# Performance work log

Hardware: AMD Instinct MI355X
Metric: run time of the kernel (lower is better)

The kernel has to match this reference:

```python
import jax, jax.numpy as jnp
import numpy as np

N, F, E, C = 50000, 128, 800000, 10

def setup_inputs() -> dict:
    key = jax.random.key(0)
    ks = jax.random.split(key, 16)
    s = 1.0 / np.sqrt(F)
    def u(k, shape):
        return jax.random.uniform(k, shape, jnp.float32, -s, s)
    inp = {
        "x": jax.random.normal(ks[0], (N, F), jnp.float32),
        "edge_index": jax.random.randint(ks[1], (2, E), 0, N),
    }
    for i, p in enumerate(["1", "2"]):
        b = 2 + i * 5
        inp["W" + p] = u(ks[b], (F, F))          # EvolveGCNO initial_weight
        inp["wih" + p] = u(ks[b + 1], (3 * F, F))  # GRU input weights (r,z,n)
        inp["whh" + p] = u(ks[b + 2], (3 * F, F))  # GRU hidden weights
        inp["bih" + p] = u(ks[b + 3], (3 * F,))
        inp["bhh" + p] = u(ks[b + 4], (3 * F,))
    inp["lin_w"] = u(ks[12], (C, F))
    inp["lin_b"] = u(ks[13], (C,))
    return inp

def gru_step(x, h, wih, whh, bih, bhh):
    # torch.nn.GRU single step; gate order r, z, n
    gi = x @ wih.T + bih
    gh = h @ whh.T + bhh
    ir, iz, inn = jnp.split(gi, 3, axis=-1)
    hr, hz, hn = jnp.split(gh, 3, axis=-1)
    r = jax.nn.sigmoid(ir + hr)
    z = jax.nn.sigmoid(iz + hz)
    n = jnp.tanh(inn + r * hn)
    return (1.0 - z) * n + z * h

def gcn_conv(W, x, src, dst):
    # GCNConv_Fixed_W: gcn_norm with self-loops, then aggregate (x @ W)
    n = x.shape[0]
    loop = jnp.arange(n)
    s = jnp.concatenate([src, loop])
    d = jnp.concatenate([dst, loop])
    deg = jax.ops.segment_sum(jnp.ones(s.shape[0], x.dtype), d, num_segments=n)
    dinv = jnp.where(deg > 0, jax.lax.rsqrt(deg), 0.0)
    norm = dinv[s] * dinv[d]                 # [E+N]
    xw = x @ W                               # [N, F]
    return jax.ops.segment_sum(norm[:, None] * xw[s], d, num_segments=n)

def evolve_gcno(x, src, dst, W0, wih, whh, bih, bhh):
    # weight evolved by GRU with input = hidden = current weight
    W = gru_step(W0, W0, wih, whh, bih, bhh)
    return gcn_conv(W, x, src, dst)

def reference(x, edge_index, W1, wih1, whh1, bih1, bhh1,
              W2, wih2, whh2, bih2, bhh2, lin_w, lin_b):
    src, dst = edge_index[0], edge_index[1]
    h = jax.nn.relu(evolve_gcno(x, src, dst, W1, wih1, whh1, bih1, bhh1))
    # dropout is identity in eval mode
    h = jax.nn.relu(evolve_gcno(h, src, dst, W2, wih2, whh2, bih2, bhh2))
    logits = h @ lin_w.T + lin_b
    return jax.nn.log_softmax(logits, axis=1)
```

## Files before the change

### kernel.cpp

```cpp
#include <hip/hip_runtime.h>
#include <cstddef>
#include <cstdint>

#define F 128
#define C_OUT 10
#define SB 256

typedef short bf16x8 __attribute__((ext_vector_type(8)));
typedef float f32x4  __attribute__((ext_vector_type(4)));
typedef float f32x2  __attribute__((ext_vector_type(2)));

__device__ __forceinline__ unsigned short bf16_rne(float f) {
  unsigned u = __float_as_uint(f);
  return (unsigned short)((u + 0x7FFFu + ((u >> 16) & 1u)) >> 16);
}

__global__ void gru_evolve2_k(const float* __restrict__ W01, const float* __restrict__ wih1,
                              const float* __restrict__ whh1, const float* __restrict__ bih1,
                              const float* __restrict__ bhh1,
                              const float* __restrict__ W02, const float* __restrict__ wih2,
                              const float* __restrict__ whh2, const float* __restrict__ bih2,
                              const float* __restrict__ bhh2,
                              unsigned short* __restrict__ Bhi1, unsigned short* __restrict__ Blo1,
                              unsigned short* __restrict__ Bhi2, unsigned short* __restrict__ Blo2,
                              int* __restrict__ counts, int n) {
  if ((int)blockIdx.x >= 128) {
    int i = ((int)blockIdx.x - 128) * SB + threadIdx.x;
    if (i < n) counts[i] = 0;
    return;
  }
  int t = blockIdx.x * 256 + threadIdx.x;
  int layer = t >> 14;
  int tt = t & 16383;
  const float* W0  = layer ? W02  : W01;
  const float* wih = layer ? wih2 : wih1;
  const float* whh = layer ? whh2 : whh1;
  const float* bih = layer ? bih2 : bih1;
  const float* bhh = layer ? bhh2 : bhh1;
  unsigned short* Bhi = layer ? Bhi2 : Bhi1;
  unsigned short* Blo = layer ? Blo2 : Blo1;
  int i = tt >> 7, j = tt & 127;
  const float4* w0r = (const float4*)(W0 + (size_t)i * F);
  float gi[3], gh[3];
#pragma unroll
  for (int g = 0; g < 3; ++g) {
    const float4* wr = (const float4*)(wih + (size_t)(g * F + j) * F);
    const float4* hr = (const float4*)(whh + (size_t)(g * F + j) * F);
    float si = 0.f, sh = 0.f;
    for (int k = 0; k < F / 4; ++k) {
      float4 a = w0r[k];
      float4 b = wr[k];
      float4 c = hr[k];
      si += a.x * b.x + a.y * b.y + a.z * b.z + a.w * b.w;
      sh += a.x * c.x + a.y * c.y + a.z * c.z + a.w * c.w;
    }
    gi[g] = si + bih[g * F + j];
    gh[g] = sh + bhh[g * F + j];
  }
  float r = 1.0f / (1.0f + expf(-(gi[0] + gh[0])));
  float z = 1.0f / (1.0f + expf(-(gi[1] + gh[1])));
  float nn = tanhf(gi[2] + r * gh[2]);
  float val = (1.0f - z) * nn + z * W0[(size_t)i * F + j];

  unsigned u = __float_as_uint(val);
  unsigned short hi = (unsigned short)(u >> 16);
  float lo_f = val - __uint_as_float(u & 0xFFFF0000u);
  unsigned short lo = bf16_rne(lo_f);
  int kstep = i >> 5, kl = i & 31;
  int lane = (kl >> 3) * 16 + (j & 15);
  int tile = j >> 4;
  int idx = ((kstep * 8 + tile) * 64 + lane) * 8 + (kl & 7);
  Bhi[idx] = hi;
  Blo[idx] = lo;
}

__global__ void count_rank_k(const int* __restrict__ dst, int* __restrict__ counts,
                             int* __restrict__ rank, int E) {
  int e = blockIdx.x * blockDim.x + threadIdx.x;
  if (e < E) rank[e] = atomicAdd(&counts[dst[e]], 1);
}

__global__ void scan_local_k(const int* __restrict__ counts, int* __restrict__ incl,
                             int* __restrict__ blocksum, int n) {
  __shared__ int sh[SB];
  int gid = blockIdx.x * SB + threadIdx.x;
  int v = (gid < n) ? counts[gid] : 0;
  sh[threadIdx.x] = v;
  __syncthreads();
  for (int off = 1; off < SB; off <<= 1) {
    int t = 0;
    if ((int)threadIdx.x >= off) t = sh[threadIdx.x - off];
    __syncthreads();
    if ((int)threadIdx.x >= off) sh[threadIdx.x] += t;
    __syncthreads();
  }
  if (gid < n) incl[gid] = sh[threadIdx.x];
  if (threadIdx.x == SB - 1) blocksum[blockIdx.x] = sh[SB - 1];
}

__global__ void scan_finish_k(const int* __restrict__ counts, const int* __restrict__ incl,
                              const int* __restrict__ blocksum, int* __restrict__ rowptr,
                              float* __restrict__ dinv, int n, int nb) {
  __shared__ int sh[SB];
  __shared__ int orig[SB];
  int v = ((int)threadIdx.x < nb) ? blocksum[threadIdx.x] : 0;
  sh[threadIdx.x] = v;
  orig[threadIdx.x] = v;
  __syncthreads();
  for (int off = 1; off < SB; off <<= 1) {
    int t = 0;
    if ((int)threadIdx.x >= off) t = sh[threadIdx.x - off];
    __syncthreads();
    if ((int)threadIdx.x >= off) sh[threadIdx.x] += t;
    __syncthreads();
  }
  int myoff = sh[blockIdx.x] - orig[blockIdx.x];
  int gid = blockIdx.x * SB + threadIdx.x;
  if (gid >= n) return;
  int c = counts[gid];
  int inc = myoff + incl[gid];
  rowptr[gid] = inc - c;
  dinv[gid] = rsqrtf((float)c + 1.0f);
  if (gid == n - 1) rowptr[n] = inc;
}

__device__ __forceinline__ void fill_body(int bid, const int* __restrict__ src,
                                          const int* __restrict__ dst,
                                          const int* __restrict__ rank,
                                          const int* __restrict__ rowptr,
                                          int* __restrict__ csr_src, int E) {
  int e = bid * 256 + (int)threadIdx.x;
  if (e < E) {
    int d = dst[e];
    csr_src[rowptr[d] + rank[e]] = src[e] << 7;
  }
}

__device__ __forceinline__ void gemm_body(int bid, const float* __restrict__ X,
                                          const unsigned short* __restrict__ Bhi,
                                          const unsigned short* __restrict__ Blo,
                                          const float* __restrict__ dinv,
                                          unsigned* __restrict__ Y, int nrows) {
  int wid = bid * 4 + ((int)threadIdx.x >> 6);
  int lane = threadIdx.x & 63;
  int ng = (nrows + 15) >> 4;
  if (wid >= ng) return;
  int g = __builtin_amdgcn_readfirstlane(wid);
  int q = lane >> 4, m = lane & 15;
  int rowA = g * 16 + m;
  if (rowA >= nrows) rowA = nrows - 1;

  f32x4 acc[8];
#pragma unroll
  for (int t = 0; t < 8; ++t) { acc[t].x = 0.f; acc[t].y = 0.f; acc[t].z = 0.f; acc[t].w = 0.f; }

#pragma unroll
  for (int s = 0; s < 4; ++s) {
    const float* xp = X + (size_t)rowA * F + s * 32 + q * 8;
    float4 xa = *(const float4*)xp;
    float4 xb = *(const float4*)(xp + 4);
    float xv[8] = {xa.x, xa.y, xa.z, xa.w, xb.x, xb.y, xb.z, xb.w};
    bf16x8 xhi, xlo;
#pragma unroll
    for (int j = 0; j < 8; ++j) {
      unsigned u = __float_as_uint(xv[j]);
      xhi[j] = (short)(u >> 16);
      float lf = xv[j] - __uint_as_float(u & 0xFFFF0000u);
      xlo[j] = (short)bf16_rne(lf);
    }
#pragma unroll
    for (int t = 0; t < 8; ++t) {
      size_t boff = ((size_t)(s * 8 + t) * 64 + lane) * 8;
      bf16x8 wh = *(const bf16x8*)(Bhi + boff);
      bf16x8 wl = *(const bf16x8*)(Blo + boff);
      acc[t] = __builtin_amdgcn_mfma_f32_16x16x32_bf16(wh, xhi, acc[t], 0, 0, 0);
      acc[t] = __builtin_amdgcn_mfma_f32_16x16x32_bf16(wh, xlo, acc[t], 0, 0, 0);
      acc[t] = __builtin_amdgcn_mfma_f32_16x16x32_bf16(wl, xhi, acc[t], 0, 0, 0);
    }
  }

  int row = g * 16 + m;
  if (row < nrows) {
    float dd = dinv[row];
    unsigned* yr = Y + (size_t)row * 32 + q;
#pragma unroll
    for (int t = 0; t < 8; ++t) {
      int p = __builtin_amdgcn_cvt_pk_fp8_f32(dd * acc[t].x, dd * acc[t].y, 0, false);
      p = __builtin_amdgcn_cvt_pk_fp8_f32(dd * acc[t].z, dd * acc[t].w, p, true);
      yr[t * 4] = (unsigned)p;
    }
  }
}

__global__ void gemm_mfma_k(const float* __restrict__ X,
                            const unsigned short* __restrict__ Bhi,
                            const unsigned short* __restrict__ Blo,
                            const float* __restrict__ dinv, unsigned* __restrict__ Y,
                            int nrows) {
  gemm_body(blockIdx.x, X, Bhi, Blo, dinv, Y, nrows);
}

__global__ void fill_gemm_k(const float* __restrict__ X,
                            const unsigned short* __restrict__ Bhi,
                            const unsigned short* __restrict__ Blo,
                            const float* __restrict__ dinv, unsigned* __restrict__ Y,
                            int nrows, int ngemm,
                            const int* __restrict__ src, const int* __restrict__ dst,
                            const int* __restrict__ rank, const int* __restrict__ rowptr,
                            int* __restrict__ csr_src, int E) {
  if ((int)blockIdx.x < ngemm)
    gemm_body(blockIdx.x, X, Bhi, Blo, dinv, Y, nrows);
  else
    fill_body((int)blockIdx.x - ngemm, src, dst, rank, rowptr, csr_src, E);
}

template <bool FUSE_LOGITS>
__global__ void agg_fp8_k(const int* __restrict__ rowptr, const int* __restrict__ csr_src,
                          const float* __restrict__ dinv, const unsigned* __restrict__ xwp,
                          float* __restrict__ hout,
                          const float* __restrict__ lw, const float* __restrict__ lb,
                          float* __restrict__ outp, int n) {
  int wave = (int)((blockIdx.x * blockDim.x + threadIdx.x) >> 6);
  int lane = threadIdx.x & 63;
  if (wave >= n) return;
  int node = __builtin_amdgcn_readfirstlane(wave);
  int half = lane >> 5, hm = lane & 31;
  float dd = dinv[node];
  const char* __restrict__ cb = (const char*)xwp;
  unsigned loff = (unsigned)(hm << 2);
  f32x2 acc0 = {0.f, 0.f}, acc1 = {0.f, 0.f};
  f32x2 bcc0 = {0.f, 0.f}, bcc1 = {0.f, 0.f};

#define DEC(U, A, B)                                           \
  do {                                                         \
    (A) += __builtin_amdgcn_cvt_pk_f32_fp8((int)(U), false);   \
    (B) += __builtin_amdgcn_cvt_pk_f32_fp8((int)(U), true);    \
  } while (0)

  {
    unsigned u = *(const unsigned*)(cb + ((((unsigned)node) << 7) | loff));
    if (half) u = 0u;
    DEC(u, acc0, acc1);
  }

  int b = rowptr[node], e = rowptr[node + 1];
  int i = b;
  for (; i + 16 <= e; i += 16) {
    int s0 = csr_src[i + 0],  s1 = csr_src[i + 1],  s2 = csr_src[i + 2],  s3 = csr_src[i + 3];
    int s4 = csr_src[i + 4],  s5 = csr_src[i + 5],  s6 = csr_src[i + 6],  s7 = csr_src[i + 7];
    int s8 = csr_src[i + 8],  s9 = csr_src[i + 9],  sA = csr_src[i + 10], sB = csr_src[i + 11];
    int sC = csr_src[i + 12], sD = csr_src[i + 13], sE = csr_src[i + 14], sF = csr_src[i + 15];
    unsigned o0 = ((unsigned)(half ? s1 : s0)) | loff;
    unsigned o1 = ((unsigned)(half ? s3 : s2)) | loff;
    unsigned o2 = ((unsigned)(half ? s5 : s4)) | loff;
    unsigned o3 = ((unsigned)(half ? s7 : s6)) | loff;
    unsigned o4 = ((unsigned)(half ? s9 : s8)) | loff;
    unsigned o5 = ((unsigned)(half ? sB : sA)) | loff;
    unsigned o6 = ((unsigned)(half ? sD : sC)) | loff;
    unsigned o7 = ((unsigned)(half ? sF : sE)) | loff;
    unsigned u0 = *(const unsigned*)(cb + o0);
    unsigned u1 = *(const unsigned*)(cb + o1);
    unsigned u2 = *(const unsigned*)(cb + o2);
    unsigned u3 = *(const unsigned*)(cb + o3);
    unsigned u4 = *(const unsigned*)(cb + o4);
    unsigned u5 = *(const unsigned*)(cb + o5);
    unsigned u6 = *(const unsigned*)(cb + o6);
    unsigned u7 = *(const unsigned*)(cb + o7);
    DEC(u0, acc0, acc1);
    DEC(u1, bcc0, bcc1);
    DEC(u2, acc0, acc1);
    DEC(u3, bcc0, bcc1);
    DEC(u4, acc0, acc1);
    DEC(u5, bcc0, bcc1);
    DEC(u6, acc0, acc1);
    DEC(u7, bcc0, bcc1);
  }
  for (; i + 8 <= e; i += 8) {
    int s0 = csr_src[i + 0], s1 = csr_src[i + 1], s2 = csr_src[i + 2], s3 = csr_src[i + 3];
    int s4 = csr_src[i + 4], s5 = csr_src[i + 5], s6 = csr_src[i + 6], s7 = csr_src[i + 7];
    unsigned o0 = ((unsigned)(half ? s1 : s0)) | loff;
    unsigned o1 = ((unsigned)(half ? s3 : s2)) | loff;
    unsigned o2 = ((unsigned)(half ? s5 : s4)) | loff;
    unsigned o3 = ((unsigned)(half ? s7 : s6)) | loff;
    unsigned u0 = *(const unsigned*)(cb + o0);
    unsigned u1 = *(const unsigned*)(cb + o1);
    unsigned u2 = *(const unsigned*)(cb + o2);
    unsigned u3 = *(const unsigned*)(cb + o3);
    DEC(u0, acc0, acc1);
    DEC(u1, bcc0, bcc1);
    DEC(u2, acc0, acc1);
    DEC(u3, bcc0, bcc1);
  }
  for (; i + 2 <= e; i += 2) {
    int s0 = csr_src[i], s1 = csr_src[i + 1];
    unsigned o = ((unsigned)(half ? s1 : s0)) | loff;
    unsigned u = *(const unsigned*)(cb + o);
    DEC(u, acc0, acc1);
  }
  if (i < e) {
    int s = csr_src[i];
    unsigned u = *(const unsigned*)(cb + (((unsigned)s) | loff));
    if (half) u = 0u;
    DEC(u, acc0, acc1);
  }
#undef DEC
  acc0 += bcc0;
  acc1 += bcc1;

  acc0.x += __shfl_xor(acc0.x, 32);
  acc0.y += __shfl_xor(acc0.y, 32);
  acc1.x += __shfl_xor(acc1.x, 32);
  acc1.y += __shfl_xor(acc1.y, 32);

  float h0 = fmaxf(dd * acc0.x, 0.f);
  float h1 = fmaxf(dd * acc0.y, 0.f);
  float h2 = fmaxf(dd * acc1.x, 0.f);
  float h3 = fmaxf(dd * acc1.y, 0.f);

  if (!FUSE_LOGITS) {
    if (half == 0) {
      *(float4*)(hout + (size_t)node * F + hm * 4) = make_float4(h0, h1, h2, h3);
    }
  } else {
    float acc[C_OUT];
#pragma unroll
    for (int c = 0; c < C_OUT; ++c) {
      float4 w = *(const float4*)(lw + (size_t)c * F + hm * 4);
      float v = h0 * w.x + h1 * w.y + h2 * w.z + h3 * w.w;
      v += __shfl_xor(v, 1); v += __shfl_xor(v, 2);
      v += __shfl_xor(v, 4); v += __shfl_xor(v, 8);
      v += __shfl_xor(v, 16);
      acc[c] = v + lb[c];
    }
    float mx = acc[0];
#pragma unroll
    for (int c = 1; c < C_OUT; ++c) mx = fmaxf(mx, acc[c]);
    float s = 0.f;
#pragma unroll
    for (int c = 0; c < C_OUT; ++c) s += expf(acc[c] - mx);
    float lse = mx + logf(s);
#pragma unroll
    for (int c = 0; c < C_OUT; ++c)
      if (lane == c) outp[(size_t)node * C_OUT + c] = acc[c] - lse;
  }
}

extern "C" void kernel_launch(void* const* d_in, const int* in_sizes, int n_in,
                              void* d_out, int out_size, void* d_ws, size_t ws_size,
                              hipStream_t stream) {
  const float* x    = (const float*)d_in[0];
  const int*   ei   = (const int*)d_in[1];
  const float* W1   = (const float*)d_in[2];
  const float* wih1 = (const float*)d_in[3];
  const float* whh1 = (const float*)d_in[4];
  const float* bih1 = (const float*)d_in[5];
  const float* bhh1 = (const float*)d_in[6];
  const float* W2   = (const float*)d_in[7];
  const float* wih2 = (const float*)d_in[8];
  const float* whh2 = (const float*)d_in[9];
  const float* bih2 = (const float*)d_in[10];
  const float* bhh2 = (const float*)d_in[11];
  const float* lw   = (const float*)d_in[12];
  const float* lb   = (const float*)d_in[13];
  float* out = (float*)d_out;

  int N = in_sizes[0] / F;
  int E = in_sizes[1] / 2;
  const int* src = ei;
  const int* dst = ei + E;
  int nb = (N + SB - 1) / SB;
  int ng = (N + 15) / 16;
  int ngemm = (ng + 3) / 4;
  int nfill = (E + 255) / 256;

  float* ws   = (float*)d_ws;
  unsigned* bufA = (unsigned*)ws;
  float* bufB = (float*)(bufA + (size_t)N * 32);
  float* dinv = bufB + (size_t)N * F;
  unsigned short* Bhi1 = (unsigned short*)(dinv + N);
  unsigned short* Blo1 = Bhi1 + F * F;
  unsigned short* Bhi2 = Blo1 + F * F;
  unsigned short* Blo2 = Bhi2 + F * F;
  int* counts = (int*)(Blo2 + F * F);
  int* rowptr = counts + N;
  int* rank   = rowptr + N + 1;
  int* incl   = rank + E;
  int* blocksum = incl + N;
  int* csr_src = blocksum + 256;

  gru_evolve2_k<<<128 + nb, 256, 0, stream>>>(W1, wih1, whh1, bih1, bhh1,
                                              W2, wih2, whh2, bih2, bhh2,
                                              Bhi1, Blo1, Bhi2, Blo2, counts, N);

  count_rank_k<<<(E + 255) / 256, 256, 0, stream>>>(dst, counts, rank, E);
  scan_local_k<<<nb, SB, 0, stream>>>(counts, incl, blocksum, N);
  scan_finish_k<<<nb, SB, 0, stream>>>(counts, incl, blocksum, rowptr, dinv, N, nb);

  fill_gemm_k<<<ngemm + nfill, 256, 0, stream>>>(x, Bhi1, Blo1, dinv, bufA, N, ngemm,
                                                 src, dst, rank, rowptr, csr_src, E);
  agg_fp8_k<false><<<(N + 3) / 4, 256, 0, stream>>>(rowptr, csr_src, dinv, bufA, bufB,
                                                    nullptr, nullptr, nullptr, N);

  gemm_mfma_k<<<ngemm, 256, 0, stream>>>(bufB, Bhi2, Blo2, dinv, bufA, N);
  agg_fp8_k<true><<<(N + 3) / 4, 256, 0, stream>>>(rowptr, csr_src, dinv, bufA, nullptr,
                                                   lw, lb, out, N);
}
```

Measured before the change: 263.5 us.

## Drop split-bf16 GEMM and split fp8 feature gather into two column-plane passes

The GEMMs now use a single bf16 MFMA per tile instead of the hi/lo three-MFMA split, and the weight lo buffers are dropped. The fp8 XW output is stored as two 64-column planes of 64 bytes per row. Each aggregation runs as two passes, one per plane, with four edges gathered per wave iteration, so each pass's gather working set is half as large and more cache-friendly. The cost is extra kernel launches, re-reading the CSR indices twice, and a partial-logit buffer round trip, plus lower GEMM precision.

```diff
diff --git a/kernel.cpp b/kernel.cpp
--- a/kernel.cpp
+++ b/kernel.cpp
@@ -21,8 +21,7 @@
                               const float* __restrict__ W02, const float* __restrict__ wih2,
                               const float* __restrict__ whh2, const float* __restrict__ bih2,
                               const float* __restrict__ bhh2,
-                              unsigned short* __restrict__ Bhi1, unsigned short* __restrict__ Blo1,
-                              unsigned short* __restrict__ Bhi2, unsigned short* __restrict__ Blo2,
+                              unsigned short* __restrict__ Bhi1, unsigned short* __restrict__ Bhi2,
                               int* __restrict__ counts, int n) {
   if ((int)blockIdx.x >= 128) {
     int i = ((int)blockIdx.x - 128) * SB + threadIdx.x;
@@ -38,7 +37,6 @@
   const float* bih = layer ? bih2 : bih1;
   const float* bhh = layer ? bhh2 : bhh1;
   unsigned short* Bhi = layer ? Bhi2 : Bhi1;
-  unsigned short* Blo = layer ? Blo2 : Blo1;
   int i = tt >> 7, j = tt & 127;
   const float4* w0r = (const float4*)(W0 + (size_t)i * F);
   float gi[3], gh[3];
@@ -62,16 +60,11 @@
   float nn = tanhf(gi[2] + r * gh[2]);
   float val = (1.0f - z) * nn + z * W0[(size_t)i * F + j];
 
-  unsigned u = __float_as_uint(val);
-  unsigned short hi = (unsigned short)(u >> 16);
-  float lo_f = val - __uint_as_float(u & 0xFFFF0000u);
-  unsigned short lo = bf16_rne(lo_f);
   int kstep = i >> 5, kl = i & 31;
   int lane = (kl >> 3) * 16 + (j & 15);
   int tile = j >> 4;
   int idx = ((kstep * 8 + tile) * 64 + lane) * 8 + (kl & 7);
-  Bhi[idx] = hi;
-  Blo[idx] = lo;
+  Bhi[idx] = bf16_rne(val);
 }
 
 __global__ void count_rank_k(const int* __restrict__ dst, int* __restrict__ counts,
@@ -132,15 +125,15 @@
   int e = bid * 256 + (int)threadIdx.x;
   if (e < E) {
     int d = dst[e];
-    csr_src[rowptr[d] + rank[e]] = src[e] << 7;
+    csr_src[rowptr[d] + rank[e]] = src[e] << 6;
   }
 }
 
 __device__ __forceinline__ void gemm_body(int bid, const float* __restrict__ X,
                                           const unsigned short* __restrict__ Bhi,
-                                          const unsigned short* __restrict__ Blo,
                                           const float* __restrict__ dinv,
-                                          unsigned* __restrict__ Y, int nrows) {
+                                          unsigned* __restrict__ Y0,
+                                          unsigned* __restrict__ Y1, int nrows) {
   int wid = bid * 4 + ((int)threadIdx.x >> 6);
   int lane = threadIdx.x & 63;
   int ng = (nrows + 15) >> 4;
@@ -160,87 +153,78 @@
     float4 xa = *(const float4*)xp;
     float4 xb = *(const float4*)(xp + 4);
     float xv[8] = {xa.x, xa.y, xa.z, xa.w, xb.x, xb.y, xb.z, xb.w};
-    bf16x8 xhi, xlo;
-#pragma unroll
-    for (int j = 0; j < 8; ++j) {
-      unsigned u = __float_as_uint(xv[j]);
-      xhi[j] = (short)(u >> 16);
-      float lf = xv[j] - __uint_as_float(u & 0xFFFF0000u);
-      xlo[j] = (short)bf16_rne(lf);
-    }
+    bf16x8 xh;
+#pragma unroll
+    for (int j = 0; j < 8; ++j) xh[j] = (short)bf16_rne(xv[j]);
 #pragma unroll
     for (int t = 0; t < 8; ++t) {
       size_t boff = ((size_t)(s * 8 + t) * 64 + lane) * 8;
       bf16x8 wh = *(const bf16x8*)(Bhi + boff);
-      bf16x8 wl = *(const bf16x8*)(Blo + boff);
-      acc[t] = __builtin_amdgcn_mfma_f32_16x16x32_bf16(wh, xhi, acc[t], 0, 0, 0);
-      acc[t] = __builtin_amdgcn_mfma_f32_16x16x32_bf16(wh, xlo, acc[t], 0, 0, 0);
-      acc[t] = __builtin_amdgcn_mfma_f32_16x16x32_bf16(wl, xhi, acc[t], 0, 0, 0);
+      acc[t] = __builtin_amdgcn_mfma_f32_16x16x32_bf16(wh, xh, acc[t], 0, 0, 0);
     }
   }
 
   int row = g * 16 + m;
   if (row < nrows) {
     float dd = dinv[row];
-    unsigned* yr = Y + (size_t)row * 32 + q;
+    unsigned* p0 = Y0 + (size_t)row * 16 + q;
+    unsigned* p1 = Y1 + (size_t)row * 16 + q;
 #pragma unroll
     for (int t = 0; t < 8; ++t) {
       int p = __builtin_amdgcn_cvt_pk_fp8_f32(dd * acc[t].x, dd * acc[t].y, 0, false);
       p = __builtin_amdgcn_cvt_pk_fp8_f32(dd * acc[t].z, dd * acc[t].w, p, true);
-      yr[t * 4] = (unsigned)p;
-    }
-  }
-}
-
-__global__ void gemm_mfma_k(const float* __restrict__ X,
-                            const unsigned short* __restrict__ Bhi,
-                            const unsigned short* __restrict__ Blo,
-                            const float* __restrict__ dinv, unsigned* __restrict__ Y,
-                            int nrows) {
-  gemm_body(blockIdx.x, X, Bhi, Blo, dinv, Y, nrows);
-}
-
-__global__ void fill_gemm_k(const float* __restrict__ X,
-                            const unsigned short* __restrict__ Bhi,
-                            const unsigned short* __restrict__ Blo,
-                            const float* __restrict__ dinv, unsigned* __restrict__ Y,
-                            int nrows, int ngemm,
+      if (t < 4) p0[(t & 3) * 4] = (unsigned)p;
+      else       p1[(t & 3) * 4] = (unsigned)p;
+    }
+  }
+}
+
+__global__ void gemm_mfma_k(const float* __restrict__ X, const unsigned short* __restrict__ Bhi,
+                            const float* __restrict__ dinv, unsigned* __restrict__ Y0,
+                            unsigned* __restrict__ Y1, int nrows) {
+  gemm_body(blockIdx.x, X, Bhi, dinv, Y0, Y1, nrows);
+}
+
+__global__ void fill_gemm_k(const float* __restrict__ X, const unsigned short* __restrict__ Bhi,
+                            const float* __restrict__ dinv, unsigned* __restrict__ Y0,
+                            unsigned* __restrict__ Y1, int nrows, int ngemm,
                             const int* __restrict__ src, const int* __restrict__ dst,
                             const int* __restrict__ rank, const int* __restrict__ rowptr,
                             int* __restrict__ csr_src, int E) {
   if ((int)blockIdx.x < ngemm)
-    gemm_body(blockIdx.x, X, Bhi, Blo, dinv, Y, nrows);
+    gemm_body(blockIdx.x, X, Bhi, dinv, Y0, Y1, nrows);
   else
     fill_body((int)blockIdx.x - ngemm, src, dst, rank, rowptr, csr_src, E);
 }
 
-template <bool FUSE_LOGITS>
-__global__ void agg_fp8_k(const int* __restrict__ rowptr, const int* __restrict__ csr_src,
-                          const float* __restrict__ dinv, const unsigned* __restrict__ xwp,
-                          float* __restrict__ hout,
-                          const float* __restrict__ lw, const float* __restrict__ lb,
-                          float* __restrict__ outp, int n) {
+template <int PASS, int MODE>
+__global__ void agg_pass_k(const int* __restrict__ rowptr, const int* __restrict__ csr_src,
+                           const float* __restrict__ dinv, const unsigned* __restrict__ plane,
+                           float* __restrict__ hout,
+                           const float* __restrict__ lw, const float* __restrict__ lb,
+                           float* __restrict__ pacc, float* __restrict__ outp, int n) {
   int wave = (int)((blockIdx.x * blockDim.x + threadIdx.x) >> 6);
   int lane = threadIdx.x & 63;
   if (wave >= n) return;
   int node = __builtin_amdgcn_readfirstlane(wave);
-  int half = lane >> 5, hm = lane & 31;
+  int m = lane & 15;
   float dd = dinv[node];
-  const char* __restrict__ cb = (const char*)xwp;
-  unsigned loff = (unsigned)(hm << 2);
-  f32x2 acc0 = {0.f, 0.f}, acc1 = {0.f, 0.f};
-  f32x2 bcc0 = {0.f, 0.f}, bcc1 = {0.f, 0.f};
-
-#define DEC(U, A, B)                                           \
-  do {                                                         \
-    (A) += __builtin_amdgcn_cvt_pk_f32_fp8((int)(U), false);   \
-    (B) += __builtin_amdgcn_cvt_pk_f32_fp8((int)(U), true);    \
+  const char* __restrict__ cb = (const char*)plane;
+  unsigned loff = (unsigned)(m << 2);
+  f32x2 a0 = {0.f, 0.f}, a1 = {0.f, 0.f};
+  f32x2 b0 = {0.f, 0.f}, b1 = {0.f, 0.f};
+
+#define SEL4(A, B, C, D) ((lane & 32) ? ((lane & 16) ? (D) : (C)) : ((lane & 16) ? (B) : (A)))
+#define DEC(U, P, Q)                                            \
+  do {                                                          \
+    (P) += __builtin_amdgcn_cvt_pk_f32_fp8((int)(U), false);    \
+    (Q) += __builtin_amdgcn_cvt_pk_f32_fp8((int)(U), true);     \
   } while (0)
 
   {
-    unsigned u = *(const unsigned*)(cb + ((((unsigned)node) << 7) | loff));
-    if (half) u = 0u;
-    DEC(u, acc0, acc1);
+    unsigned u = *(const unsigned*)(cb + ((((unsigned)node) << 6) | loff));
+    if (lane >= 16) u = 0u;
+    DEC(u, a0, a1);
   }
 
   int b = rowptr[node], e = rowptr[node + 1];
@@ -250,98 +234,78 @@
     int s4 = csr_src[i + 4],  s5 = csr_src[i + 5],  s6 = csr_src[i + 6],  s7 = csr_src[i + 7];
     int s8 = csr_src[i + 8],  s9 = csr_src[i + 9],  sA = csr_src[i + 10], sB = csr_src[i + 11];
     int sC = csr_src[i + 12], sD = csr_src[i + 13], sE = csr_src[i + 14], sF = csr_src[i + 15];
-    unsigned o0 = ((unsigned)(half ? s1 : s0)) | loff;
-    unsigned o1 = ((unsigned)(half ? s3 : s2)) | loff;
-    unsigned o2 = ((unsigned)(half ? s5 : s4)) | loff;
-    unsigned o3 = ((unsigned)(half ? s7 : s6)) | loff;
-    unsigned o4 = ((unsigned)(half ? s9 : s8)) | loff;
-    unsigned o5 = ((unsigned)(half ? sB : sA)) | loff;
-    unsigned o6 = ((unsigned)(half ? sD : sC)) | loff;
-    unsigned o7 = ((unsigned)(half ? sF : sE)) | loff;
+    unsigned o0 = ((unsigned)SEL4(s0, s1, s2, s3)) | loff;
+    unsigned o1 = ((unsigned)SEL4(s4, s5, s6, s7)) | loff;
+    unsigned o2 = ((unsigned)SEL4(s8, s9, sA, sB)) | loff;
+    unsigned o3 = ((unsigned)SEL4(sC, sD, sE, sF)) | loff;
     unsigned u0 = *(const unsigned*)(cb + o0);
     unsigned u1 = *(const unsigned*)(cb + o1);
     unsigned u2 = *(const unsigned*)(cb + o2);
     unsigned u3 = *(const unsigned*)(cb + o3);
-    unsigned u4 = *(const unsigned*)(cb + o4);
-    unsigned u5 = *(const unsigned*)(cb + o5);
-    unsigned u6 = *(const unsigned*)(cb + o6);
-    unsigned u7 = *(const unsigned*)(cb + o7);
-    DEC(u0, acc0, acc1);
-    DEC(u1, bcc0, bcc1);
-    DEC(u2, acc0, acc1);
-    DEC(u3, bcc0, bcc1);
-    DEC(u4, acc0, acc1);
-    DEC(u5, bcc0, bcc1);
-    DEC(u6, acc0, acc1);
-    DEC(u7, bcc0, bcc1);
-  }
-  for (; i + 8 <= e; i += 8) {
-    int s0 = csr_src[i + 0], s1 = csr_src[i + 1], s2 = csr_src[i + 2], s3 = csr_src[i + 3];
-    int s4 = csr_src[i + 4], s5 = csr_src[i + 5], s6 = csr_src[i + 6], s7 = csr_src[i + 7];
-    unsigned o0 = ((unsigned)(half ? s1 : s0)) | loff;
-    unsigned o1 = ((unsigned)(half ? s3 : s2)) | loff;
-    unsigned o2 = ((unsigned)(half ? s5 : s4)) | loff;
-    unsigned o3 = ((unsigned)(half ? s7 : s6)) | loff;
-    unsigned u0 = *(const unsigned*)(cb + o0);
-    unsigned u1 = *(const unsigned*)(cb + o1);
-    unsigned u2 = *(const unsigned*)(cb + o2);
-    unsigned u3 = *(const unsigned*)(cb + o3);
-    DEC(u0, acc0, acc1);
-    DEC(u1, bcc0, bcc1);
-    DEC(u2, acc0, acc1);
-    DEC(u3, bcc0, bcc1);
-  }
-  for (; i + 2 <= e; i += 2) {
-    int s0 = csr_src[i], s1 = csr_src[i + 1];
-    unsigned o = ((unsigned)(half ? s1 : s0)) | loff;
+    DEC(u0, a0, a1);
+    DEC(u1, b0, b1);
+    DEC(u2, a0, a1);
+    DEC(u3, b0, b1);
+  }
+  for (; i < e; i += 4) {
+    int e1 = e - 1;
+    int c1 = (i + 1 < e) ? i + 1 : e1;
+    int c2 = (i + 2 < e) ? i + 2 : e1;
+    int c3 = (i + 3 < e) ? i + 3 : e1;
+    int s0 = csr_src[i], s1 = csr_src[c1], s2 = csr_src[c2], s3 = csr_src[c3];
+    unsigned o = ((unsigned)SEL4(s0, s1, s2, s3)) | loff;
     unsigned u = *(const unsigned*)(cb + o);
-    DEC(u, acc0, acc1);
-  }
-  if (i < e) {
-    int s = csr_src[i];
-    unsigned u = *(const unsigned*)(cb + (((unsigned)s) | loff));
-    if (half) u = 0u;
-    DEC(u, acc0, acc1);
+    int idx = i + (lane >> 4);
+    if (idx >= e) u = 0u;
+    DEC(u, a0, a1);
   }
 #undef DEC
-  acc0 += bcc0;
-  acc1 += bcc1;
-
-  acc0.x += __shfl_xor(acc0.x, 32);
-  acc0.y += __shfl_xor(acc0.y, 32);
-  acc1.x += __shfl_xor(acc1.x, 32);
-  acc1.y += __shfl_xor(acc1.y, 32);
-
-  float h0 = fmaxf(dd * acc0.x, 0.f);
-  float h1 = fmaxf(dd * acc0.y, 0.f);
-  float h2 = fmaxf(dd * acc1.x, 0.f);
-  float h3 = fmaxf(dd * acc1.y, 0.f);
-
-  if (!FUSE_LOGITS) {
-    if (half == 0) {
-      *(float4*)(hout + (size_t)node * F + hm * 4) = make_float4(h0, h1, h2, h3);
-    }
+#undef SEL4
+  a0 += b0;
+  a1 += b1;
+
+  a0.x += __shfl_xor(a0.x, 16); a0.y += __shfl_xor(a0.y, 16);
+  a1.x += __shfl_xor(a1.x, 16); a1.y += __shfl_xor(a1.y, 16);
+  a0.x += __shfl_xor(a0.x, 32); a0.y += __shfl_xor(a0.y, 32);
+  a1.x += __shfl_xor(a1.x, 32); a1.y += __shfl_xor(a1.y, 32);
+
+  float h0 = fmaxf(dd * a0.x, 0.f);
+  float h1 = fmaxf(dd * a0.y, 0.f);
+  float h2 = fmaxf(dd * a1.x, 0.f);
+  float h3 = fmaxf(dd * a1.y, 0.f);
+
+  if (MODE == 0) {
+    if (lane < 16)
+      *(float4*)(hout + (size_t)node * F + PASS * 64 + m * 4) = make_float4(h0, h1, h2, h3);
   } else {
     float acc[C_OUT];
 #pragma unroll
     for (int c = 0; c < C_OUT; ++c) {
-      float4 w = *(const float4*)(lw + (size_t)c * F + hm * 4);
+      float4 w = *(const float4*)(lw + (size_t)c * F + PASS * 64 + m * 4);
       float v = h0 * w.x + h1 * w.y + h2 * w.z + h3 * w.w;
       v += __shfl_xor(v, 1); v += __shfl_xor(v, 2);
       v += __shfl_xor(v, 4); v += __shfl_xor(v, 8);
-      v += __shfl_xor(v, 16);
-      acc[c] = v + lb[c];
-    }
-    float mx = acc[0];
-#pragma unroll
-    for (int c = 1; c < C_OUT; ++c) mx = fmaxf(mx, acc[c]);
-    float s = 0.f;
-#pragma unroll
-    for (int c = 0; c < C_OUT; ++c) s += expf(acc[c] - mx);
-    float lse = mx + logf(s);
-#pragma unroll
-    for (int c = 0; c < C_OUT; ++c)
-      if (lane == c) outp[(size_t)node * C_OUT + c] = acc[c] - lse;
+      acc[c] = v;
+    }
+    if (MODE == 1) {
+#pragma unroll
+      for (int c = 0; c < C_OUT; ++c)
+        if (lane == c) pacc[(size_t)node * C_OUT + c] = acc[c];
+    } else {
+#pragma unroll
+      for (int c = 0; c < C_OUT; ++c)
+        acc[c] += pacc[(size_t)node * C_OUT + c] + lb[c];
+      float mx = acc[0];
+#pragma unroll
+      for (int c = 1; c < C_OUT; ++c) mx = fmaxf(mx, acc[c]);
+      float s = 0.f;
+#pragma unroll
+      for (int c = 0; c < C_OUT; ++c) s += expf(acc[c] - mx);
+      float lse = mx + logf(s);
+#pragma unroll
+      for (int c = 0; c < C_OUT; ++c)
+        if (lane == c) outp[(size_t)node * C_OUT + c] = acc[c] - lse;
+    }
   }
 }
 
@@ -372,36 +336,41 @@
   int ng = (N + 15) / 16;
   int ngemm = (ng + 3) / 4;
   int nfill = (E + 255) / 256;
-
-  float* ws   = (float*)d_ws;
-  unsigned* bufA = (unsigned*)ws;
-  float* bufB = (float*)(bufA + (size_t)N * 32);
+  int nagg = (N + 3) / 4;
+
+  float* ws = (float*)d_ws;
+  unsigned* plane0 = (unsigned*)ws;
+  unsigned* plane1 = plane0 + (size_t)N * 16;
+  float* bufB = (float*)(plane1 + (size_t)N * 16);
   float* dinv = bufB + (size_t)N * F;
   unsigned short* Bhi1 = (unsigned short*)(dinv + N);
-  unsigned short* Blo1 = Bhi1 + F * F;
-  unsigned short* Bhi2 = Blo1 + F * F;
-  unsigned short* Blo2 = Bhi2 + F * F;
-  int* counts = (int*)(Blo2 + F * F);
+  unsigned short* Bhi2 = Bhi1 + F * F;
+  int* counts = (int*)(Bhi2 + F * F);
   int* rowptr = counts + N;
   int* rank   = rowptr + N + 1;
   int* incl   = rank + E;
   int* blocksum = incl + N;
   int* csr_src = blocksum + 256;
+  float* pacc = (float*)(csr_src + E);
 
   gru_evolve2_k<<<128 + nb, 256, 0, stream>>>(W1, wih1, whh1, bih1, bhh1,
                                               W2, wih2, whh2, bih2, bhh2,
-                                              Bhi1, Blo1, Bhi2, Blo2, counts, N);
+                                              Bhi1, Bhi2, counts, N);
 
   count_rank_k<<<(E + 255) / 256, 256, 0, stream>>>(dst, counts, rank, E);
   scan_local_k<<<nb, SB, 0, stream>>>(counts, incl, blocksum, N);
   scan_finish_k<<<nb, SB, 0, stream>>>(counts, incl, blocksum, rowptr, dinv, N, nb);
 
-  fill_gemm_k<<<ngemm + nfill, 256, 0, stream>>>(x, Bhi1, Blo1, dinv, bufA, N, ngemm,
+  fill_gemm_k<<<ngemm + nfill, 256, 0, stream>>>(x, Bhi1, dinv, plane0, plane1, N, ngemm,
                                                  src, dst, rank, rowptr, csr_src, E);
-  agg_fp8_k<false><<<(N + 3) / 4, 256, 0, stream>>>(rowptr, csr_src, dinv, bufA, bufB,
-                                                    nullptr, nullptr, nullptr, N);
-
-  gemm_mfma_k<<<ngemm, 256, 0, stream>>>(bufB, Bhi2, Blo2, dinv, bufA, N);
-  agg_fp8_k<true><<<(N + 3) / 4, 256, 0, stream>>>(rowptr, csr_src, dinv, bufA, nullptr,
-                                                   lw, lb, out, N);
-}
+  agg_pass_k<0, 0><<<nagg, 256, 0, stream>>>(rowptr, csr_src, dinv, plane0, bufB,
+                                             nullptr, nullptr, nullptr, nullptr, N);
+  agg_pass_k<1, 0><<<nagg, 256, 0, stream>>>(rowptr, csr_src, dinv, plane1, bufB,
+                                             nullptr, nullptr, nullptr, nullptr, N);
+
+  gemm_mfma_k<<<ngemm, 256, 0, stream>>>(bufB, Bhi2, dinv, plane0, plane1, N);
+  agg_pass_k<0, 1><<<nagg, 256, 0, stream>>>(rowptr, csr_src, dinv, plane0, nullptr,
+                                             lw, lb, pacc, nullptr, N);
+  agg_pass_k<1, 2><<<nagg, 256, 0, stream>>>(rowptr, csr_src, dinv, plane1, nullptr,
+                                             lw, lb, pacc, out, N);
+}
```

Result: slower. 314.6 us (+19.4%).
